# Performance work log

Hardware: AMD Instinct MI355X
Metric: run time of the kernel (lower is better)

## Reference

```python
import jax, jax.numpy as jnp
import numpy as np

B, S, D_IN, D = 8, 4096, 512, 256


def setup_inputs() -> dict:
    key = jax.random.key(0)
    ks = jax.random.split(key, 7)
    s_in = 1.0 / np.sqrt(D_IN)
    return {
        "x": jax.random.normal(ks[0], (B, S, D_IN), dtype=jnp.float32),
        "Wq": jax.random.normal(ks[1], (D_IN, D), dtype=jnp.float32) * s_in,
        "bq": jnp.zeros((D,), dtype=jnp.float32),
        "Wk": jax.random.normal(ks[2], (D_IN, D), dtype=jnp.float32) * s_in,
        "bk": jnp.zeros((D,), dtype=jnp.float32),
        "Wv": jax.random.normal(ks[3], (D_IN, D), dtype=jnp.float32) * s_in,
        "bv": jnp.zeros((D,), dtype=jnp.float32),
    }


def reference(x, Wq, bq, Wk, bk, Wv, bv):
    # Q/K/V projections (three Dense layers in the original)
    Q = jnp.einsum("bsd,de->bse", x, Wq) + bq  # [B,S,D]
    K = jnp.einsum("bsd,de->bse", x, Wk) + bk
    V = jnp.einsum("bsd,de->bse", x, Wv) + bv
    # scaled dot-product attention: softmax(QK^T / sqrt(d)) V
    scale = 1.0 / jnp.sqrt(jnp.asarray(Q.shape[-1], dtype=Q.dtype))
    scores = jnp.einsum("bqe,bke->bqk", Q, K) * scale  # [B,S,S]
    attn = jax.nn.softmax(scores, axis=-1)
    out = jnp.einsum("bqk,bke->bqe", attn, V)  # [B,S,D]
    return out
```

## Files before the change

### kernel.cpp

```cpp
#include <hip/hip_runtime.h>
#include <hip/hip_bf16.h>
#include <stdint.h>

#define B_   8
#define S_   4096
#define DIN  512
#define D_   256
#define ROWS (B_ * S_)

typedef __attribute__((ext_vector_type(8))) short short8;
typedef __attribute__((ext_vector_type(4))) float floatx4;
typedef __attribute__((ext_vector_type(16))) float floatx16;
typedef __attribute__((ext_vector_type(4))) short short4v;
typedef __attribute__((ext_vector_type(2))) unsigned uint2v;

__device__ __forceinline__ void gll16(const void* g, void* lds) {
  __builtin_amdgcn_global_load_lds(
      (const __attribute__((address_space(1))) void*)g,
      (__attribute__((address_space(3))) void*)lds, 16, 0, 0);
}
__device__ __forceinline__ short f2bf(float x) {
  union { float f; unsigned u; } c; c.f = x;
  unsigned r = (c.u + 0x7FFF + ((c.u >> 16) & 1)) >> 16;
  return (short)r;
}
__device__ __forceinline__ float bf2f(short v) {
  union { unsigned u; float f; } c; c.u = ((unsigned)(unsigned short)v) << 16;
  return c.f;
}
__device__ __forceinline__ unsigned pk2bf(float a, float b) {
  union { __hip_bfloat162 h; unsigned u; } c;
  c.h = __float22bfloat162_rn(float2{a, b});
  return c.u;
}
__device__ __forceinline__ float fexp2(float x) {
#if __has_builtin(__builtin_amdgcn_exp2f)
  return __builtin_amdgcn_exp2f(x);
#else
  return exp2f(x);
#endif
}

__device__ __forceinline__ void plswap(unsigned& a, unsigned& b, int H) {
#if __has_builtin(__builtin_amdgcn_permlane32_swap)
  uint2v r = __builtin_amdgcn_permlane32_swap(a, b, false, false);
  a = r[0]; b = r[1];
#else
  unsigned sa = (unsigned)__shfl_xor((int)a, 32);
  unsigned sb = (unsigned)__shfl_xor((int)b, 32);
  unsigned na = H ? sb : a;
  unsigned nb = H ? b : sa;
  a = na; b = nb;
#endif
}

__global__ __launch_bounds__(256) void detect_kernel(
    const unsigned short* __restrict__ w, int* __restrict__ flag) {
  const int tid = threadIdx.x;
  float m = 0.f;
#pragma unroll
  for (int j = 0; j < 16; ++j) {
    float f = bf2f((short)w[tid * 16 + j]);
    m = fmaxf(m, fabsf(f));
  }
#pragma unroll
  for (int d = 1; d < 64; d <<= 1) m = fmaxf(m, __shfl_xor(m, d));
  __shared__ float red[4];
  if ((tid & 63) == 0) red[tid >> 6] = m;
  __syncthreads();
  if (tid == 0) {
    float mm = fmaxf(fmaxf(red[0], red[1]), fmaxf(red[2], red[3]));
    flag[0] = (mm > 1000.0f) ? 1 : 0;
  }
}

__global__ __launch_bounds__(256) void cvt_kernel(
    const void* __restrict__ src, short* __restrict__ dst, int n,
    const int* __restrict__ flag) {
  const int i = blockIdx.x * 256 + threadIdx.x;
  if (i * 4 >= n) return;
  if (*flag) {
    float4 v = ((const float4*)src)[i];
    short4v o;
    o[0] = f2bf(v.x); o[1] = f2bf(v.y); o[2] = f2bf(v.z); o[3] = f2bf(v.w);
    ((short4v*)dst)[i] = o;
  } else {
    ((short4v*)dst)[i] = ((const short4v*)src)[i];
  }
}

__global__ __launch_bounds__(256) void wtcvt_kernel(
    const void* __restrict__ Wq, const void* __restrict__ Wk,
    const void* __restrict__ Wv, short* __restrict__ Wt,
    const int* __restrict__ flag) {
  __shared__ float tile[32][33];
  const int mat = blockIdx.z;
  const void* W = (mat == 0) ? Wq : ((mat == 1) ? Wk : Wv);
  const int n0 = blockIdx.x * 32, k0 = blockIdx.y * 32;
  const int tx = threadIdx.x & 31, ty = threadIdx.x >> 5;
  const bool f32 = (*flag != 0);
#pragma unroll
  for (int i = 0; i < 4; ++i) {
    int k = ty + i * 8;
    float v = f32 ? ((const float*)W)[(k0 + k) * D_ + n0 + tx]
                  : bf2f(((const short*)W)[(k0 + k) * D_ + n0 + tx]);
    tile[k][tx] = v;
  }
  __syncthreads();
  short* o = Wt + mat * (D_ * DIN);
#pragma unroll
  for (int i = 0; i < 4; ++i) {
    int n = ty + i * 8;
    o[(n0 + n) * DIN + k0 + tx] = f2bf(tile[tx][n]);
  }
}

__global__ __launch_bounds__(256) void biascvt_kernel(
    const void* __restrict__ bq, const void* __restrict__ bk,
    const void* __restrict__ bv, short* __restrict__ bbuf,
    const int* __restrict__ flag) {
  const int tid = threadIdx.x;
  const bool f32 = (*flag != 0);
  const void* p[3] = {bq, bk, bv};
#pragma unroll
  for (int m = 0; m < 3; ++m)
    bbuf[m * D_ + tid] = f32 ? f2bf(((const float*)p[m])[tid])
                             : ((const short*)p[m])[tid];
}

__global__ __launch_bounds__(256, 2) void qkv_kernel(
    const short* __restrict__ x, const short* __restrict__ Wt,
    const short* __restrict__ bb,
    short* __restrict__ Qg, short* __restrict__ Kg, short* __restrict__ Vtg) {
  __shared__ short As[2][512 * 8];
  __shared__ short Bs[2][512 * 8];
  const int tid = threadIdx.x;
  const int lane = tid & 63, w = tid >> 6;
  const int li = lane & 15, g = lane >> 4;
  const int mb = blockIdx.x;
  const int mat = blockIdx.y >> 1, nb = blockIdx.y & 1;
  const short* Ag = x + mb * 128 * DIN;
  const short* Bt = Wt + mat * (D_ * DIN) + nb * 128 * DIN;

  auto stage = [&](int buf, int k0) {
#pragma unroll
    for (int p = 0; p < 2; ++p) {
      int c = p * 256 + tid;
      int row = c >> 2, og = (c & 3) ^ (row & 3);
      gll16(Ag + row * DIN + k0 + og * 8, &As[buf][(p * 256 + w * 64) * 8]);
    }
#pragma unroll
    for (int p = 0; p < 2; ++p) {
      int c = p * 256 + tid;
      int row = c >> 2, og = (c & 3) ^ (row & 3);
      gll16(Bt + row * DIN + k0 + og * 8, &Bs[buf][(p * 256 + w * 64) * 8]);
    }
  };

  const int msub = (w & 1) * 64, nsub = (w >> 1) * 64;
  floatx4 acc[4][4];
#pragma unroll
  for (int i = 0; i < 4; ++i)
#pragma unroll
    for (int j = 0; j < 4; ++j) acc[i][j] = floatx4{0.f, 0.f, 0.f, 0.f};

  stage(0, 0);
  __syncthreads();
  for (int kt = 0; kt < 16; ++kt) {
    if (kt < 15) stage((kt + 1) & 1, (kt + 1) * 32);
    const int buf = kt & 1;
    short8 af[4], bfr[4];
#pragma unroll
    for (int mt = 0; mt < 4; ++mt) {
      int row = msub + mt * 16 + li;
      int og = g ^ (row & 3);
      af[mt] = *(const short8*)&As[buf][(row * 4 + og) * 8];
    }
#pragma unroll
    for (int nt = 0; nt < 4; ++nt) {
      int row = nsub + nt * 16 + li;
      int og = g ^ (row & 3);
      bfr[nt] = *(const short8*)&Bs[buf][(row * 4 + og) * 8];
    }
#pragma unroll
    for (int mt = 0; mt < 4; ++mt)
#pragma unroll
      for (int nt = 0; nt < 4; ++nt)
        acc[mt][nt] = __builtin_amdgcn_mfma_f32_16x16x32_bf16(
            af[mt], bfr[nt], acc[mt][nt], 0, 0, 0);
    __syncthreads();
  }

  const short* bias = bb + mat * 256;
  if (mat < 2) {
    short* O = (mat == 0) ? Qg : Kg;
#pragma unroll
    for (int nt = 0; nt < 4; ++nt) {
      float bv_ = bf2f(bias[nb * 128 + nsub + nt * 16 + li]);
#pragma unroll
      for (int mt = 0; mt < 4; ++mt)
#pragma unroll
        for (int r = 0; r < 4; ++r) {
          int m = mb * 128 + msub + mt * 16 + g * 4 + r;
          int n = nb * 128 + nsub + nt * 16 + li;
          O[m * D_ + n] = f2bf(acc[mt][nt][r] + bv_);
        }
    }
  } else {
#pragma unroll
    for (int nt = 0; nt < 4; ++nt) {
      float bv_ = bf2f(bias[nb * 128 + nsub + nt * 16 + li]);
#pragma unroll
      for (int mt = 0; mt < 4; ++mt) {
        int m0 = mb * 128 + msub + mt * 16 + g * 4;
        int batch = m0 >> 12, s = m0 & (S_ - 1);
        int n = nb * 128 + nsub + nt * 16 + li;
        short4v pk;
#pragma unroll
        for (int r = 0; r < 4; ++r) pk[r] = f2bf(acc[mt][nt][r] + bv_);
        *(short4v*)&Vtg[(batch * D_ + n) * S_ + s] = pk;
      }
    }
  }
}

__global__ __launch_bounds__(256, 2) void attn_kernel(
    const short* __restrict__ Qg, const short* __restrict__ Kg,
    const short* __restrict__ Vtg, short* __restrict__ Op,
    float* __restrict__ lsum) {
  __shared__ short Ks[2][1024 * 8];
  __shared__ short Vs[2][1024 * 8];
  const int tid = threadIdx.x, lane = tid & 63, w = tid >> 6;
  const int q = lane & 31, H = lane >> 5;
  const int id = blockIdx.x;
  const int bb = id & 7;
  const int h = (id >> 3) & 1;
  const int q0 = (id >> 4) * 128;
  const int qrow = q0 + w * 32;
  const int s_base = h * 2048;

  const short* Qb = Qg + (size_t)(bb * S_ + qrow) * D_;
  const short* Kb = Kg + (size_t)bb * S_ * D_;
  const short* Vb = Vtg + (size_t)bb * D_ * S_;

  short8 qf[16];
#pragma unroll
  for (int o = 0; o < 16; ++o)
    qf[o] = *(const short8*)&Qb[q * D_ + o * 16 + H * 8];

  floatx16 oa[8];
#pragma unroll
  for (int n2 = 0; n2 < 8; ++n2)
#pragma unroll
    for (int i = 0; i < 16; ++i) oa[n2][i] = 0.f;
  float lst = 0.f;

  auto stage = [&](int t, int buf) {
    const int s0 = s_base + t * 32;
#pragma unroll
    for (int p = 0; p < 4; ++p) {
      int c = p * 256 + tid;
      int s = c >> 5, od = (c & 31) ^ s;
      gll16(&Kb[(s0 + s) * D_ + od * 8], &Ks[buf][c * 8]);
    }
#pragma unroll
    for (int p = 0; p < 4; ++p) {
      int c = p * 256 + tid;
      int e = c >> 2, so = (c & 3) ^ ((e >> 1) & 3);
      gll16(&Vb[e * S_ + s0 + so * 8], &Vs[buf][c * 8]);
    }
  };

  const float cs = 0.09016844005556f;
  const float M12 = 12.0f;
  stage(0, 0);
  __syncthreads();

  for (int t = 0; t < 64; ++t) {
    if (t < 63) stage(t + 1, (t + 1) & 1);
    const int buf = t & 1;

    floatx16 sc0, sc1;
#pragma unroll
    for (int i = 0; i < 16; ++i) { sc0[i] = 0.f; sc1[i] = 0.f; }
    __builtin_amdgcn_s_setprio(1);
#pragma unroll
    for (int o = 0; o < 16; o += 2) {
      short8 kf0 = *(const short8*)&Ks[buf][(q * 32 + ((2 * o + H) ^ q)) * 8];
      short8 kf1 =
          *(const short8*)&Ks[buf][(q * 32 + ((2 * (o + 1) + H) ^ q)) * 8];
      sc0 = __builtin_amdgcn_mfma_f32_32x32x16_bf16(kf0, qf[o], sc0, 0, 0, 0);
      sc1 =
          __builtin_amdgcn_mfma_f32_32x32x16_bf16(kf1, qf[o + 1], sc1, 0, 0, 0);
    }
    __builtin_amdgcn_s_setprio(0);
#pragma unroll
    for (int i = 0; i < 16; ++i) sc0[i] += sc1[i];

    float t8[8];
#pragma unroll
    for (int hh = 0; hh < 2; ++hh) {
      float pvv[8];
#pragma unroll
      for (int i = 0; i < 8; ++i)
        pvv[i] = fexp2(sc0[8 * hh + i] * cs - M12);
      unsigned dwv[4];
#pragma unroll
      for (int m = 0; m < 4; ++m) dwv[m] = pk2bf(pvv[2 * m], pvv[2 * m + 1]);
#pragma unroll
      for (int m = 0; m < 4; ++m) t8[4 * hh + m] = pvv[2 * m] + pvv[2 * m + 1];
      plswap(dwv[0], dwv[2], H);
      plswap(dwv[1], dwv[3], H);
      union { unsigned u[4]; short8 s; } pk_;
      pk_.u[0] = dwv[0]; pk_.u[1] = dwv[1]; pk_.u[2] = dwv[2];
      pk_.u[3] = dwv[3];
      short8 pfrh = pk_.s;

      __builtin_amdgcn_s_setprio(1);
#pragma unroll
      for (int n2 = 0; n2 < 8; ++n2) {
        const int e = n2 * 32 + q;
        const int esw = (e >> 1) & 3;
        short8 vf =
            *(const short8*)&Vs[buf][(e * 4 + ((2 * hh + H) ^ esw)) * 8];
        oa[n2] = __builtin_amdgcn_mfma_f32_32x32x16_bf16(vf, pfrh, oa[n2],
                                                         0, 0, 0);
      }
      __builtin_amdgcn_s_setprio(0);
    }

    float t4[4];
#pragma unroll
    for (int m = 0; m < 4; ++m) t4[m] = t8[2 * m] + t8[2 * m + 1];
    float rs = (t4[0] + t4[1]) + (t4[2] + t4[3]);
    rs += __shfl_xor(rs, 32);
    lst += rs;

    __syncthreads();
  }

  const float inv = 1.0f / lst;
  short* Oh = Op + (size_t)h * ROWS * D_ + (size_t)(bb * S_ + qrow) * D_;
#pragma unroll
  for (int n2 = 0; n2 < 8; ++n2) {
#pragma unroll
    for (int qd = 0; qd < 4; ++qd) {
      int e0 = n2 * 32 + 8 * qd + 4 * H;
      uint2v st;
      st[0] = pk2bf(oa[n2][4 * qd] * inv, oa[n2][4 * qd + 1] * inv);
      st[1] = pk2bf(oa[n2][4 * qd + 2] * inv, oa[n2][4 * qd + 3] * inv);
      *(uint2v*)&Oh[q * D_ + e0] = st;
    }
  }
  if (H == 0) {
    int grow = bb * S_ + qrow + q;
    lsum[h * ROWS + grow] = lst;
  }
}

__global__ __launch_bounds__(256) void combine_kernel(
    const short* __restrict__ Op, const float* __restrict__ lsum,
    void* __restrict__ outv, const int* __restrict__ flag) {
  const int gid = blockIdx.x * 256 + threadIdx.x;
  const int row = gid >> 6;
  const int e4 = (gid & 63) * 4;
  const float l1 = lsum[row], l2 = lsum[ROWS + row];
  const float inv = 1.0f / (l1 + l2);
  const float c1 = l1 * inv, c2 = l2 * inv;
  short4v a = *(const short4v*)&Op[(size_t)row * D_ + e4];
  short4v b = *(const short4v*)&Op[(size_t)(ROWS + row) * D_ + e4];
  if (*flag) {
    float4 o;
    o.x = c1 * bf2f(a[0]) + c2 * bf2f(b[0]);
    o.y = c1 * bf2f(a[1]) + c2 * bf2f(b[1]);
    o.z = c1 * bf2f(a[2]) + c2 * bf2f(b[2]);
    o.w = c1 * bf2f(a[3]) + c2 * bf2f(b[3]);
    *(float4*)&((float*)outv)[(size_t)row * D_ + e4] = o;
  } else {
    short4v o;
#pragma unroll
    for (int j = 0; j < 4; ++j)
      o[j] = f2bf(c1 * bf2f(a[j]) + c2 * bf2f(b[j]));
    *(short4v*)&((short*)outv)[(size_t)row * D_ + e4] = o;
  }
}

extern "C" void kernel_launch(void* const* d_in, const int* in_sizes, int n_in,
                              void* d_out, int out_size, void* d_ws, size_t ws_size,
                              hipStream_t stream) {
  const void* x  = d_in[0];
  const void* Wq = d_in[1];
  const void* bq = d_in[2];
  const void* Wk = d_in[3];
  const void* bk = d_in[4];
  const void* Wv = d_in[5];
  const void* bv = d_in[6];
  char* ws = (char*)d_ws;
  int*   flag = (int*)(ws);
  short* bbuf = (short*)(ws + 256);
  float* lsum = (float*)(ws + 4096);
  short* Wt   = (short*)(ws + (1u << 20));
  short* xb   = (short*)(ws + (2u << 20));
  short* Qw   = (short*)(ws + (34u << 20));
  short* Kw   = (short*)(ws + (50u << 20));
  short* Vtw  = (short*)(ws + (66u << 20));
  short* Op   = xb;

  hipLaunchKernelGGL(detect_kernel, dim3(1), dim3(256), 0, stream,
                     (const unsigned short*)Wq, flag);
  hipLaunchKernelGGL(cvt_kernel, dim3(16384), dim3(256), 0, stream,
                     x, xb, B_ * S_ * DIN, flag);
  hipLaunchKernelGGL(wtcvt_kernel, dim3(8, 16, 3), dim3(256), 0, stream,
                     Wq, Wk, Wv, Wt, flag);
  hipLaunchKernelGGL(biascvt_kernel, dim3(1), dim3(256), 0, stream,
                     bq, bk, bv, bbuf, flag);
  hipLaunchKernelGGL(qkv_kernel, dim3(256, 6), dim3(256), 0, stream,
                     xb, Wt, bbuf, Qw, Kw, Vtw);
  hipLaunchKernelGGL(attn_kernel, dim3(512), dim3(256), 0, stream,
                     Qw, Kw, Vtw, Op, lsum);
  hipLaunchKernelGGL(combine_kernel, dim3(ROWS / 4), dim3(256), 0, stream,
                     Op, lsum, d_out, flag);
}
```

Before: 371.4 us.

## Single-buffer V and prefetch K two tiles ahead with manual vmcnt waits

The attention loop now keeps K double-buffered but prefetched two tiles ahead, while V is single-buffered and loaded for the next tile right after the PV MMAs finish. Explicit s_waitcnt vmcnt counts and raw barriers replace __syncthreads, so the first softmax half can overlap with the V load before waiting. This cuts LDS use (which may allow more occupancy) and tries to hide load latency better. In exchange there are more barriers per iteration and fragile hand-counted vmcnt values that must match the number of issued loads.

```diff
diff --git a/kernel.cpp b/kernel.cpp
--- a/kernel.cpp
+++ b/kernel.cpp
@@ -53,6 +53,13 @@
   a = na; b = nb;
 #endif
 }
+
+#define ASM_VMCNT(N) asm volatile("s_waitcnt vmcnt(" #N ")" ::: "memory")
+#define BARRIER()                      \
+  do {                                 \
+    __builtin_amdgcn_s_barrier();      \
+    __builtin_amdgcn_sched_barrier(0); \
+  } while (0)
 
 __global__ __launch_bounds__(256) void detect_kernel(
     const unsigned short* __restrict__ w, int* __restrict__ flag) {
@@ -229,7 +236,7 @@
     const short* __restrict__ Vtg, short* __restrict__ Op,
     float* __restrict__ lsum) {
   __shared__ short Ks[2][1024 * 8];
-  __shared__ short Vs[2][1024 * 8];
+  __shared__ short Vs[1024 * 8];
   const int tid = threadIdx.x, lane = tid & 63, w = tid >> 6;
   const int q = lane & 31, H = lane >> 5;
   const int id = blockIdx.x;
@@ -255,7 +262,7 @@
     for (int i = 0; i < 16; ++i) oa[n2][i] = 0.f;
   float lst = 0.f;
 
-  auto stage = [&](int t, int buf) {
+  auto stageK = [&](int t, int buf) {
     const int s0 = s_base + t * 32;
 #pragma unroll
     for (int p = 0; p < 4; ++p) {
@@ -263,21 +270,27 @@
       int s = c >> 5, od = (c & 31) ^ s;
       gll16(&Kb[(s0 + s) * D_ + od * 8], &Ks[buf][c * 8]);
     }
+  };
+  auto stageV = [&](int t) {
+    const int s0 = s_base + t * 32;
 #pragma unroll
     for (int p = 0; p < 4; ++p) {
       int c = p * 256 + tid;
       int e = c >> 2, so = (c & 3) ^ ((e >> 1) & 3);
-      gll16(&Vb[e * S_ + s0 + so * 8], &Vs[buf][c * 8]);
+      gll16(&Vb[e * S_ + s0 + so * 8], &Vs[c * 8]);
     }
   };
 
   const float cs = 0.09016844005556f;
   const float M12 = 12.0f;
-  stage(0, 0);
-  __syncthreads();
+
+  stageK(0, 0);
+  stageV(0);
+  stageK(1, 1);
+  ASM_VMCNT(8);
+  BARRIER();
 
   for (int t = 0; t < 64; ++t) {
-    if (t < 63) stage(t + 1, (t + 1) & 1);
     const int buf = t & 1;
 
     floatx16 sc0, sc1;
@@ -298,36 +311,58 @@
     for (int i = 0; i < 16; ++i) sc0[i] += sc1[i];
 
     float t8[8];
-#pragma unroll
-    for (int hh = 0; hh < 2; ++hh) {
-      float pvv[8];
-#pragma unroll
-      for (int i = 0; i < 8; ++i)
-        pvv[i] = fexp2(sc0[8 * hh + i] * cs - M12);
-      unsigned dwv[4];
-#pragma unroll
-      for (int m = 0; m < 4; ++m) dwv[m] = pk2bf(pvv[2 * m], pvv[2 * m + 1]);
-#pragma unroll
-      for (int m = 0; m < 4; ++m) t8[4 * hh + m] = pvv[2 * m] + pvv[2 * m + 1];
-      plswap(dwv[0], dwv[2], H);
-      plswap(dwv[1], dwv[3], H);
-      union { unsigned u[4]; short8 s; } pk_;
-      pk_.u[0] = dwv[0]; pk_.u[1] = dwv[1]; pk_.u[2] = dwv[2];
-      pk_.u[3] = dwv[3];
-      short8 pfrh = pk_.s;
-
-      __builtin_amdgcn_s_setprio(1);
-#pragma unroll
-      for (int n2 = 0; n2 < 8; ++n2) {
-        const int e = n2 * 32 + q;
-        const int esw = (e >> 1) & 3;
-        short8 vf =
-            *(const short8*)&Vs[buf][(e * 4 + ((2 * hh + H) ^ esw)) * 8];
-        oa[n2] = __builtin_amdgcn_mfma_f32_32x32x16_bf16(vf, pfrh, oa[n2],
-                                                         0, 0, 0);
-      }
-      __builtin_amdgcn_s_setprio(0);
-    }
+    float pv0[8];
+#pragma unroll
+    for (int i = 0; i < 8; ++i) pv0[i] = fexp2(sc0[i] * cs - M12);
+    unsigned dw0[4];
+#pragma unroll
+    for (int m = 0; m < 4; ++m) dw0[m] = pk2bf(pv0[2 * m], pv0[2 * m + 1]);
+#pragma unroll
+    for (int m = 0; m < 4; ++m) t8[m] = pv0[2 * m] + pv0[2 * m + 1];
+    plswap(dw0[0], dw0[2], H);
+    plswap(dw0[1], dw0[3], H);
+    union { unsigned u[4]; short8 s; } pk0;
+    pk0.u[0] = dw0[0]; pk0.u[1] = dw0[1]; pk0.u[2] = dw0[2]; pk0.u[3] = dw0[3];
+    short8 pfr0 = pk0.s;
+
+    if (t < 63) { ASM_VMCNT(4); } else { ASM_VMCNT(0); }
+    BARRIER();
+
+    __builtin_amdgcn_s_setprio(1);
+#pragma unroll
+    for (int n2 = 0; n2 < 8; ++n2) {
+      const int e = n2 * 32 + q;
+      const int esw = (e >> 1) & 3;
+      short8 vf = *(const short8*)&Vs[(e * 4 + ((2 * 0 + H) ^ esw)) * 8];
+      oa[n2] =
+          __builtin_amdgcn_mfma_f32_32x32x16_bf16(vf, pfr0, oa[n2], 0, 0, 0);
+    }
+    __builtin_amdgcn_s_setprio(0);
+
+    float pv1[8];
+#pragma unroll
+    for (int i = 0; i < 8; ++i) pv1[i] = fexp2(sc0[8 + i] * cs - M12);
+    unsigned dw1[4];
+#pragma unroll
+    for (int m = 0; m < 4; ++m) dw1[m] = pk2bf(pv1[2 * m], pv1[2 * m + 1]);
+#pragma unroll
+    for (int m = 0; m < 4; ++m) t8[4 + m] = pv1[2 * m] + pv1[2 * m + 1];
+    plswap(dw1[0], dw1[2], H);
+    plswap(dw1[1], dw1[3], H);
+    union { unsigned u[4]; short8 s; } pk1;
+    pk1.u[0] = dw1[0]; pk1.u[1] = dw1[1]; pk1.u[2] = dw1[2]; pk1.u[3] = dw1[3];
+    short8 pfr1 = pk1.s;
+
+    __builtin_amdgcn_s_setprio(1);
+#pragma unroll
+    for (int n2 = 0; n2 < 8; ++n2) {
+      const int e = n2 * 32 + q;
+      const int esw = (e >> 1) & 3;
+      short8 vf = *(const short8*)&Vs[(e * 4 + ((2 * 1 + H) ^ esw)) * 8];
+      oa[n2] =
+          __builtin_amdgcn_mfma_f32_32x32x16_bf16(vf, pfr1, oa[n2], 0, 0, 0);
+    }
+    __builtin_amdgcn_s_setprio(0);
 
     float t4[4];
 #pragma unroll
@@ -336,7 +371,16 @@
     rs += __shfl_xor(rs, 32);
     lst += rs;
 
-    __syncthreads();
+    BARRIER();
+    if (t < 63) stageV(t + 1);
+    if (t < 62) stageK(t + 2, buf);
+    if (t < 62) {
+      ASM_VMCNT(8);
+      BARRIER();
+    } else if (t == 62) {
+      ASM_VMCNT(4);
+      BARRIER();
+    }
   }
 
   const float inv = 1.0f / lst;
```

New measurement: 459.1 us. +23.6%, slower.
